# Optimization experiments

Measured on AMD Instinct MI355X. Metric: run time of the kernel, lower is better.

The kernel has to match this reference:

```python
import jax, jax.numpy as jnp
import numpy as np

IN_C = 128
HID = 128
LEAF = 50000
N0, W = 100000, 16
N1, N2 = 25000, 5000
E1, E2 = 500000, 100000


def setup_inputs() -> dict:
    key = jax.random.key(0)
    ks = jax.random.split(key, 16)
    emb = jax.random.normal(ks[0], (LEAF, IN_C), jnp.float32) * 0.02
    emb = emb.at[0].set(0.0)  # padding_idx=0
    inp = {
        "x": jax.random.randint(ks[1], (N0, W), 0, LEAF),
        "src1": jax.random.randint(ks[2], (E1,), 0, N0),
        "dst1": jax.random.randint(ks[3], (E1,), 0, N1),
        "src2": jax.random.randint(ks[4], (E2,), 0, N1),
        "dst2": jax.random.randint(ks[5], (E2,), 0, N2),
        "n1": N1,
        "n2": N2,
        "emb": emb,
        "ln_g": jnp.ones((IN_C,), jnp.float32),
        "ln_b": jnp.zeros((IN_C,), jnp.float32),
        "Wl1": jax.random.normal(ks[6], (HID, IN_C), jnp.float32) * 0.05,
        "bl1": jnp.zeros((HID,), jnp.float32),
        "Wr1": jax.random.normal(ks[7], (HID, IN_C), jnp.float32) * 0.05,
        "Wl2": jax.random.normal(ks[8], (HID, HID), jnp.float32) * 0.05,
        "bl2": jnp.zeros((HID,), jnp.float32),
        "Wr2": jax.random.normal(ks[9], (HID, HID), jnp.float32) * 0.05,
    }
    return inp


def _layernorm(h, g, b, eps=1e-5):
    mu = jnp.mean(h, axis=-1, keepdims=True)
    var = jnp.mean(jnp.square(h - mu), axis=-1, keepdims=True)
    return (h - mu) * jax.lax.rsqrt(var + eps) * g + b


def _sage_conv(h, src, dst, n_tgt, Wl, bl, Wr):
    # bipartite SAGEConv with mean aggregation (PyG default):
    # out = lin_l(mean_j h[src_j -> i]) + lin_r(h[:n_tgt])
    msg = h[src]  # [E, C] irregular gather
    agg = jax.ops.segment_sum(msg, dst, num_segments=n_tgt)
    cnt = jax.ops.segment_sum(jnp.ones((src.shape[0],), h.dtype), dst, num_segments=n_tgt)
    mean = agg / jnp.maximum(cnt, 1.0)[:, None]
    return mean @ Wl.T + bl + h[:n_tgt] @ Wr.T


def reference(x, src1, dst1, src2, dst2, n1, n2, emb, ln_g, ln_b,
              Wl1, bl1, Wr1, Wl2, bl2, Wr2):
    h = jnp.sum(emb[x], axis=1)               # [N0, C] embedding-bag sum
    h = jax.nn.relu(_layernorm(h, ln_g, ln_b))
    h = _sage_conv(h, src1, dst1, n1, Wl1, bl1, Wr1)
    h = jax.nn.relu(h)                        # dropout: eval mode -> identity
    h = _sage_conv(h, src2, dst2, n2, Wl2, bl2, Wr2)
    return h
```

## Files before the change

### kernel.cpp

```cpp
#include <hip/hip_runtime.h>

#define C 128
#define LDSPAD 136
#define CAP 64

typedef unsigned int uint;
typedef unsigned short ushort;
typedef __attribute__((ext_vector_type(8))) short bf16x8;
typedef __attribute__((ext_vector_type(4))) float f32x4;

__device__ __forceinline__ float bf_lo(uint u) { return __uint_as_float(u << 16); }
__device__ __forceinline__ float bf_hi(uint u) { return __uint_as_float(u & 0xffff0000u); }
__device__ __forceinline__ uint f2bf(float f) {
  uint u = __float_as_uint(f);
  return (u + 0x7fffu + ((u >> 16) & 1u)) >> 16;
}

__global__ __launch_bounds__(256) void k_prep(
    const float4* __restrict__ emb, ushort4* __restrict__ embh, int n4,
    const float4* __restrict__ w0, const float4* __restrict__ w1,
    const float4* __restrict__ w2, const float4* __restrict__ w3,
    ushort4* __restrict__ wb, int nw4each,
    int4* __restrict__ zb, int nz4) {
  int i = blockIdx.x * blockDim.x + threadIdx.x;
  if (i < n4) {
    float4 f = emb[i];
    ushort4 o = {(ushort)f2bf(f.x), (ushort)f2bf(f.y), (ushort)f2bf(f.z), (ushort)f2bf(f.w)};
    embh[i] = o;
  }
  if (i < 4 * nw4each) {
    int m = i / nw4each;
    int j = i - m * nw4each;
    const float4* w = (m == 0) ? w0 : (m == 1) ? w1 : (m == 2) ? w2 : w3;
    float4 f = w[j];
    ushort4 o = {(ushort)f2bf(f.x), (ushort)f2bf(f.y), (ushort)f2bf(f.z), (ushort)f2bf(f.w)};
    wb[i] = o;
  }
  if (i < nz4) {
    int4 z = {0, 0, 0, 0};
    zb[i] = z;
  }
}

__global__ __launch_bounds__(256) void k_embed_bucket(
    const int* __restrict__ x, const ushort* __restrict__ emb,
    const float* __restrict__ g, const float* __restrict__ b,
    ushort* __restrict__ h, int n0,
    const int* __restrict__ src1, const int* __restrict__ dst1,
    int* __restrict__ cnt1, int* __restrict__ slots1, int e1,
    const int* __restrict__ src2, const int* __restrict__ dst2,
    int* __restrict__ cnt2, int* __restrict__ slots2, int e2,
    int bucketBlocks) {
  if (blockIdx.x < bucketBlocks) {
    int i = blockIdx.x * blockDim.x + threadIdx.x;
    if (i < e1) {
      int d = dst1[i];
      int p = atomicAdd(&cnt1[d], 1);
      if (p < CAP) slots1[d * CAP + p] = src1[i];
    } else if (i < e1 + e2) {
      int j = i - e1;
      int d = dst2[j];
      int p = atomicAdd(&cnt2[d], 1);
      if (p < CAP) slots2[d * CAP + p] = src2[j];
    }
    return;
  }
  int node = (blockIdx.x - bucketBlocks) * 4 + (threadIdx.x >> 6);
  int lane = threadIdx.x & 63;
  if (node >= n0) return;
  int grp = lane >> 5, sub = lane & 31;
  int xv = x[(size_t)node * 16 + (lane & 15)];
  float s0 = 0.f, s1 = 0.f, s2 = 0.f, s3 = 0.f;
#pragma unroll
  for (int w = 0; w < 16; w += 2) {
    int tok = __shfl(xv, w + grp, 64);
    uint2 u = ((const uint2*)(emb + (size_t)tok * C))[sub];
    s0 += bf_lo(u.x); s1 += bf_hi(u.x); s2 += bf_lo(u.y); s3 += bf_hi(u.y);
  }
  s0 += __shfl_xor(s0, 32, 64);
  s1 += __shfl_xor(s1, 32, 64);
  s2 += __shfl_xor(s2, 32, 64);
  s3 += __shfl_xor(s3, 32, 64);
  float red = s0 + s1 + s2 + s3;
#pragma unroll
  for (int off = 16; off; off >>= 1) red += __shfl_xor(red, off, 64);
  float mu = red * (1.f / C);
  float c0 = s0 - mu, c1 = s1 - mu, c2 = s2 - mu, c3 = s3 - mu;
  float sq = c0 * c0 + c1 * c1 + c2 * c2 + c3 * c3;
#pragma unroll
  for (int off = 16; off; off >>= 1) sq += __shfl_xor(sq, off, 64);
  float rs = rsqrtf(sq * (1.f / C) + 1e-5f);
  float4 gg = ((const float4*)g)[sub];
  float4 bb = ((const float4*)b)[sub];
  float o0 = fmaxf(c0 * rs * gg.x + bb.x, 0.f);
  float o1 = fmaxf(c1 * rs * gg.y + bb.y, 0.f);
  float o2 = fmaxf(c2 * rs * gg.z + bb.z, 0.f);
  float o3 = fmaxf(c3 * rs * gg.w + bb.w, 0.f);
  if (grp == 0) {
    ushort4 o = {(ushort)f2bf(o0), (ushort)f2bf(o1), (ushort)f2bf(o2), (ushort)f2bf(o3)};
    ((ushort4*)(h + (size_t)node * C))[sub] = o;
  }
}

template <bool RELU, bool BF16OUT>
__global__ __launch_bounds__(512) void k_conv(
    const int* __restrict__ cntArr, const int* __restrict__ slots,
    const ushort* __restrict__ h, const ushort* __restrict__ Wlb,
    const float* __restrict__ bl, const ushort* __restrict__ Wrb,
    void* __restrict__ outp, int ntgt) {
  __shared__ ushort smean[16 * LDSPAD];
  int wave = threadIdx.x >> 6;
  int lane = threadIdx.x & 63;
  int grp = lane >> 5, sub = lane & 31;
  int mbase = blockIdx.x * 16;
  int nl = wave * 2 + grp;
  int node = mbase + nl;

  int truecnt = (node < ntgt) ? cntArr[node] : 0;
  int cnt = min(truecnt, CAP);
  const int* sl = slots + (size_t)(node < ntgt ? node : 0) * CAP;
  int ev = (sub < cnt) ? sl[sub] : 0;
  int ev2 = (sub + 32 < cnt) ? sl[sub + 32] : 0;
  int dmax = max(cnt, __shfl_xor(cnt, 32, 64));
  int half = grp * 32;
  float s0 = 0.f, s1 = 0.f, s2 = 0.f, s3 = 0.f;
  for (int d = 0; d < dmax; d += 8) {
#pragma unroll
    for (int k = 0; k < 8; ++k) {
      int dk = d + k;
      int e = (dk < 32) ? __shfl(ev, half + dk, 64) : __shfl(ev2, half + dk - 32, 64);
      uint2 u = ((const uint2*)(h + (size_t)e * C))[sub];
      uint msk = (dk < cnt) ? 0xffffffffu : 0u;
      u.x &= msk; u.y &= msk;
      s0 += bf_lo(u.x); s1 += bf_hi(u.x); s2 += bf_lo(u.y); s3 += bf_hi(u.y);
    }
  }
  float sc = 1.f / (float)max(truecnt, 1);
  ushort4 o = {(ushort)f2bf(s0 * sc), (ushort)f2bf(s1 * sc),
               (ushort)f2bf(s2 * sc), (ushort)f2bf(s3 * sc)};
  *(ushort4*)(smean + nl * LDSPAD + sub * 4) = o;
  __syncthreads();

  int r16 = lane & 15;
  int quad = lane >> 4;
  int koff = quad * 8;
  bf16x8 am[4], ah[4];
  int hr = min(mbase + r16, ntgt - 1);
  const ushort* hrow = h + (size_t)hr * C;
#pragma unroll
  for (int kc = 0; kc < 4; ++kc) {
    am[kc] = *(const bf16x8*)(smean + r16 * LDSPAD + kc * 32 + koff);
    ah[kc] = *(const bf16x8*)(hrow + kc * 32 + koff);
  }
  int nbase = wave * 16;
  float bias = bl[nbase + r16];
  f32x4 acc = {bias, bias, bias, bias};
  const ushort* wlrow = Wlb + (size_t)(nbase + r16) * C;
  const ushort* wrrow = Wrb + (size_t)(nbase + r16) * C;
#pragma unroll
  for (int kc = 0; kc < 4; ++kc) {
    bf16x8 wl = *(const bf16x8*)(wlrow + kc * 32 + koff);
    acc = __builtin_amdgcn_mfma_f32_16x16x32_bf16(am[kc], wl, acc, 0, 0, 0);
    bf16x8 wr = *(const bf16x8*)(wrrow + kc * 32 + koff);
    acc = __builtin_amdgcn_mfma_f32_16x16x32_bf16(ah[kc], wr, acc, 0, 0, 0);
  }
#pragma unroll
  for (int r = 0; r < 4; ++r) {
    int row = mbase + quad * 4 + r;
    if (row < ntgt) {
      float v = acc[r];
      if (RELU) v = fmaxf(v, 0.f);
      if (BF16OUT)
        ((ushort*)outp)[(size_t)row * C + nbase + r16] = (ushort)f2bf(v);
      else
        ((float*)outp)[(size_t)row * C + nbase + r16] = v;
    }
  }
}

extern "C" void kernel_launch(void* const* d_in, const int* in_sizes, int n_in,
                              void* d_out, int out_size, void* d_ws, size_t ws_size,
                              hipStream_t stream) {
  const int*   x    = (const int*)d_in[0];
  const int*   src1 = (const int*)d_in[1];
  const int*   dst1 = (const int*)d_in[2];
  const int*   src2 = (const int*)d_in[3];
  const int*   dst2 = (const int*)d_in[4];
  const float* emb  = (const float*)d_in[7];
  const float* ln_g = (const float*)d_in[8];
  const float* ln_b = (const float*)d_in[9];
  const float* Wl1  = (const float*)d_in[10];
  const float* bl1  = (const float*)d_in[11];
  const float* Wr1  = (const float*)d_in[12];
  const float* Wl2  = (const float*)d_in[13];
  const float* bl2  = (const float*)d_in[14];
  const float* Wr2  = (const float*)d_in[15];

  const int N0 = in_sizes[0] / 16;
  const int E1 = in_sizes[1];
  const int E2 = in_sizes[3];
  const int N1 = 25000;
  const int N2 = 5000;
  const int LEAF_ELEMS = in_sizes[7];
  const int W_ELEMS = C * C;

  char* ws = (char*)d_ws;
  size_t off = 0;
  auto alloc = [&](size_t bytes) {
    char* p = ws + off;
    off += (bytes + 255) & ~(size_t)255;
    return p;
  };
  ushort* embh   = (ushort*)alloc((size_t)LEAF_ELEMS * 2);
  ushort* h0     = (ushort*)alloc((size_t)N0 * C * 2);
  ushort* h1     = (ushort*)alloc((size_t)N1 * C * 2);
  ushort* wb     = (ushort*)alloc((size_t)4 * W_ELEMS * 2);
  int*    slots1 = (int*)alloc((size_t)N1 * CAP * 4);
  int*    slots2 = (int*)alloc((size_t)N2 * CAP * 4);
  char*   zbase  = ws + off;
  int*    cnt1   = (int*)alloc((size_t)N1 * 4);
  int*    cnt2   = (int*)alloc((size_t)N2 * 4);
  size_t  zbytes = (size_t)((ws + off) - zbase);

  float* out = (float*)d_out;
  ushort* Wl1b = wb;
  ushort* Wr1b = wb + W_ELEMS;
  ushort* Wl2b = wb + 2 * W_ELEMS;
  ushort* Wr2b = wb + 3 * W_ELEMS;

  {
    int n4 = LEAF_ELEMS / 4;
    int nw4each = W_ELEMS / 4;
    int nz4 = (int)(zbytes / 16);
    k_prep<<<(n4 + 255) / 256, 256, 0, stream>>>(
        (const float4*)emb, (ushort4*)embh, n4,
        (const float4*)Wl1, (const float4*)Wr1, (const float4*)Wl2, (const float4*)Wr2,
        (ushort4*)wb, nw4each, (int4*)zbase, nz4);
  }

  {
    int bucketBlocks = (E1 + E2 + 255) / 256;
    int embBlocks = (N0 + 3) / 4;
    k_embed_bucket<<<bucketBlocks + embBlocks, 256, 0, stream>>>(
        x, embh, ln_g, ln_b, h0, N0,
        src1, dst1, cnt1, slots1, E1,
        src2, dst2, cnt2, slots2, E2, bucketBlocks);
  }

  k_conv<true, true><<<(N1 + 15) / 16, 512, 0, stream>>>(
      cnt1, slots1, h0, Wl1b, bl1, Wr1b, h1, N1);

  k_conv<false, false><<<(N2 + 15) / 16, 512, 0, stream>>>(
      cnt2, slots2, h1, Wl2b, bl2, Wr2b, out, N2);
}
```

Before: 230.9 us.

## Fuse all stages into one persistent cooperative kernel with grid syncs

Replaces the four separate launches (prep, embed+bucket, two convs) with a single cooperative persistent kernel that uses grid-stride loops and grid.sync between phases. This removes per-launch overhead and inter-kernel gaps. It also makes the edge bucketing and the embedding phase share the same threads instead of separate blocks. The cost is grid-wide barriers, occupancy capped by launch bounds, and a host occupancy query on every call.

```diff
diff --git a/kernel.cpp b/kernel.cpp
--- a/kernel.cpp
+++ b/kernel.cpp
@@ -1,4 +1,7 @@
 #include <hip/hip_runtime.h>
+#include <hip/hip_cooperative_groups.h>
+
+namespace cg = cooperative_groups;
 
 #define C 128
 #define LDSPAD 136
@@ -16,240 +19,252 @@
   return (u + 0x7fffu + ((u >> 16) & 1u)) >> 16;
 }
 
-__global__ __launch_bounds__(256) void k_prep(
-    const float4* __restrict__ emb, ushort4* __restrict__ embh, int n4,
-    const float4* __restrict__ w0, const float4* __restrict__ w1,
-    const float4* __restrict__ w2, const float4* __restrict__ w3,
-    ushort4* __restrict__ wb, int nw4each,
-    int4* __restrict__ zb, int nz4) {
-  int i = blockIdx.x * blockDim.x + threadIdx.x;
-  if (i < n4) {
-    float4 f = emb[i];
-    ushort4 o = {(ushort)f2bf(f.x), (ushort)f2bf(f.y), (ushort)f2bf(f.z), (ushort)f2bf(f.w)};
-    embh[i] = o;
-  }
-  if (i < 4 * nw4each) {
-    int m = i / nw4each;
-    int j = i - m * nw4each;
-    const float4* w = (m == 0) ? w0 : (m == 1) ? w1 : (m == 2) ? w2 : w3;
-    float4 f = w[j];
-    ushort4 o = {(ushort)f2bf(f.x), (ushort)f2bf(f.y), (ushort)f2bf(f.z), (ushort)f2bf(f.w)};
-    wb[i] = o;
-  }
-  if (i < nz4) {
-    int4 z = {0, 0, 0, 0};
-    zb[i] = z;
-  }
-}
-
-__global__ __launch_bounds__(256) void k_embed_bucket(
-    const int* __restrict__ x, const ushort* __restrict__ emb,
-    const float* __restrict__ g, const float* __restrict__ b,
-    ushort* __restrict__ h, int n0,
-    const int* __restrict__ src1, const int* __restrict__ dst1,
-    int* __restrict__ cnt1, int* __restrict__ slots1, int e1,
-    const int* __restrict__ src2, const int* __restrict__ dst2,
-    int* __restrict__ cnt2, int* __restrict__ slots2, int e2,
-    int bucketBlocks) {
-  if (blockIdx.x < bucketBlocks) {
-    int i = blockIdx.x * blockDim.x + threadIdx.x;
-    if (i < e1) {
-      int d = dst1[i];
-      int p = atomicAdd(&cnt1[d], 1);
-      if (p < CAP) slots1[d * CAP + p] = src1[i];
-    } else if (i < e1 + e2) {
-      int j = i - e1;
-      int d = dst2[j];
-      int p = atomicAdd(&cnt2[d], 1);
-      if (p < CAP) slots2[d * CAP + p] = src2[j];
-    }
-    return;
-  }
-  int node = (blockIdx.x - bucketBlocks) * 4 + (threadIdx.x >> 6);
-  int lane = threadIdx.x & 63;
-  if (node >= n0) return;
-  int grp = lane >> 5, sub = lane & 31;
-  int xv = x[(size_t)node * 16 + (lane & 15)];
-  float s0 = 0.f, s1 = 0.f, s2 = 0.f, s3 = 0.f;
-#pragma unroll
-  for (int w = 0; w < 16; w += 2) {
-    int tok = __shfl(xv, w + grp, 64);
-    uint2 u = ((const uint2*)(emb + (size_t)tok * C))[sub];
-    s0 += bf_lo(u.x); s1 += bf_hi(u.x); s2 += bf_lo(u.y); s3 += bf_hi(u.y);
-  }
-  s0 += __shfl_xor(s0, 32, 64);
-  s1 += __shfl_xor(s1, 32, 64);
-  s2 += __shfl_xor(s2, 32, 64);
-  s3 += __shfl_xor(s3, 32, 64);
-  float red = s0 + s1 + s2 + s3;
-#pragma unroll
-  for (int off = 16; off; off >>= 1) red += __shfl_xor(red, off, 64);
-  float mu = red * (1.f / C);
-  float c0 = s0 - mu, c1 = s1 - mu, c2 = s2 - mu, c3 = s3 - mu;
-  float sq = c0 * c0 + c1 * c1 + c2 * c2 + c3 * c3;
-#pragma unroll
-  for (int off = 16; off; off >>= 1) sq += __shfl_xor(sq, off, 64);
-  float rs = rsqrtf(sq * (1.f / C) + 1e-5f);
-  float4 gg = ((const float4*)g)[sub];
-  float4 bb = ((const float4*)b)[sub];
-  float o0 = fmaxf(c0 * rs * gg.x + bb.x, 0.f);
-  float o1 = fmaxf(c1 * rs * gg.y + bb.y, 0.f);
-  float o2 = fmaxf(c2 * rs * gg.z + bb.z, 0.f);
-  float o3 = fmaxf(c3 * rs * gg.w + bb.w, 0.f);
-  if (grp == 0) {
-    ushort4 o = {(ushort)f2bf(o0), (ushort)f2bf(o1), (ushort)f2bf(o2), (ushort)f2bf(o3)};
-    ((ushort4*)(h + (size_t)node * C))[sub] = o;
-  }
-}
+struct Params {
+  const int* x;
+  const float* emb;
+  const float* ln_g;
+  const float* ln_b;
+  const int* src1; const int* dst1;
+  const int* src2; const int* dst2;
+  const float* Wl1; const float* bl1; const float* Wr1;
+  const float* Wl2; const float* bl2; const float* Wr2;
+  ushort* embh; ushort* h0; ushort* h1; ushort* wb;
+  int* cnt1; int* slots1; int* cnt2; int* slots2;
+  int4* zbase; int nz4;
+  float* out;
+  int n0, e1, e2, n1, n2, leafElems;
+};
 
 template <bool RELU, bool BF16OUT>
-__global__ __launch_bounds__(512) void k_conv(
+__device__ __forceinline__ void conv_phase(
     const int* __restrict__ cntArr, const int* __restrict__ slots,
     const ushort* __restrict__ h, const ushort* __restrict__ Wlb,
     const float* __restrict__ bl, const ushort* __restrict__ Wrb,
-    void* __restrict__ outp, int ntgt) {
-  __shared__ ushort smean[16 * LDSPAD];
+    void* __restrict__ outp, int ntgt, ushort* smean) {
   int wave = threadIdx.x >> 6;
   int lane = threadIdx.x & 63;
   int grp = lane >> 5, sub = lane & 31;
-  int mbase = blockIdx.x * 16;
-  int nl = wave * 2 + grp;
-  int node = mbase + nl;
-
-  int truecnt = (node < ntgt) ? cntArr[node] : 0;
-  int cnt = min(truecnt, CAP);
-  const int* sl = slots + (size_t)(node < ntgt ? node : 0) * CAP;
-  int ev = (sub < cnt) ? sl[sub] : 0;
-  int ev2 = (sub + 32 < cnt) ? sl[sub + 32] : 0;
-  int dmax = max(cnt, __shfl_xor(cnt, 32, 64));
-  int half = grp * 32;
-  float s0 = 0.f, s1 = 0.f, s2 = 0.f, s3 = 0.f;
-  for (int d = 0; d < dmax; d += 8) {
-#pragma unroll
-    for (int k = 0; k < 8; ++k) {
-      int dk = d + k;
-      int e = (dk < 32) ? __shfl(ev, half + dk, 64) : __shfl(ev2, half + dk - 32, 64);
-      uint2 u = ((const uint2*)(h + (size_t)e * C))[sub];
-      uint msk = (dk < cnt) ? 0xffffffffu : 0u;
-      u.x &= msk; u.y &= msk;
-      s0 += bf_lo(u.x); s1 += bf_hi(u.x); s2 += bf_lo(u.y); s3 += bf_hi(u.y);
-    }
-  }
-  float sc = 1.f / (float)max(truecnt, 1);
-  ushort4 o = {(ushort)f2bf(s0 * sc), (ushort)f2bf(s1 * sc),
-               (ushort)f2bf(s2 * sc), (ushort)f2bf(s3 * sc)};
-  *(ushort4*)(smean + nl * LDSPAD + sub * 4) = o;
-  __syncthreads();
-
   int r16 = lane & 15;
   int quad = lane >> 4;
   int koff = quad * 8;
-  bf16x8 am[4], ah[4];
-  int hr = min(mbase + r16, ntgt - 1);
-  const ushort* hrow = h + (size_t)hr * C;
-#pragma unroll
-  for (int kc = 0; kc < 4; ++kc) {
-    am[kc] = *(const bf16x8*)(smean + r16 * LDSPAD + kc * 32 + koff);
-    ah[kc] = *(const bf16x8*)(hrow + kc * 32 + koff);
+  int ntiles = (ntgt + 15) >> 4;
+  for (int t = blockIdx.x; t < ntiles; t += gridDim.x) {
+    int mbase = t * 16;
+    int nl = wave * 2 + grp;
+    int node = mbase + nl;
+    __syncthreads();
+    int truecnt = (node < ntgt) ? cntArr[node] : 0;
+    int cnt = min(truecnt, CAP);
+    const int* sl = slots + (size_t)(node < ntgt ? node : 0) * CAP;
+    int ev = (sub < cnt) ? sl[sub] : 0;
+    int ev2 = (sub + 32 < cnt) ? sl[sub + 32] : 0;
+    int dmax = max(cnt, __shfl_xor(cnt, 32, 64));
+    int half = grp * 32;
+    float s0 = 0.f, s1 = 0.f, s2 = 0.f, s3 = 0.f;
+    for (int d = 0; d < dmax; d += 8) {
+#pragma unroll
+      for (int k = 0; k < 8; ++k) {
+        int dk = d + k;
+        int e = (dk < 32) ? __shfl(ev, half + dk, 64) : __shfl(ev2, half + dk - 32, 64);
+        uint2 u = ((const uint2*)(h + (size_t)e * C))[sub];
+        uint msk = (dk < cnt) ? 0xffffffffu : 0u;
+        u.x &= msk; u.y &= msk;
+        s0 += bf_lo(u.x); s1 += bf_hi(u.x); s2 += bf_lo(u.y); s3 += bf_hi(u.y);
+      }
+    }
+    float sc = 1.f / (float)max(truecnt, 1);
+    ushort4 o = {(ushort)f2bf(s0 * sc), (ushort)f2bf(s1 * sc),
+                 (ushort)f2bf(s2 * sc), (ushort)f2bf(s3 * sc)};
+    *(ushort4*)(smean + nl * LDSPAD + sub * 4) = o;
+    __syncthreads();
+    bf16x8 am[4], ah[4];
+    int hr = min(mbase + r16, ntgt - 1);
+    const ushort* hrow = h + (size_t)hr * C;
+#pragma unroll
+    for (int kc = 0; kc < 4; ++kc) {
+      am[kc] = *(const bf16x8*)(smean + r16 * LDSPAD + kc * 32 + koff);
+      ah[kc] = *(const bf16x8*)(hrow + kc * 32 + koff);
+    }
+    int nbase = wave * 16;
+    float bias = bl[nbase + r16];
+    f32x4 acc = {bias, bias, bias, bias};
+    const ushort* wlrow = Wlb + (size_t)(nbase + r16) * C;
+    const ushort* wrrow = Wrb + (size_t)(nbase + r16) * C;
+#pragma unroll
+    for (int kc = 0; kc < 4; ++kc) {
+      bf16x8 wl = *(const bf16x8*)(wlrow + kc * 32 + koff);
+      acc = __builtin_amdgcn_mfma_f32_16x16x32_bf16(am[kc], wl, acc, 0, 0, 0);
+      bf16x8 wr = *(const bf16x8*)(wrrow + kc * 32 + koff);
+      acc = __builtin_amdgcn_mfma_f32_16x16x32_bf16(ah[kc], wr, acc, 0, 0, 0);
+    }
+#pragma unroll
+    for (int r = 0; r < 4; ++r) {
+      int row = mbase + quad * 4 + r;
+      if (row < ntgt) {
+        float v = acc[r];
+        if (RELU) v = fmaxf(v, 0.f);
+        if (BF16OUT)
+          ((ushort*)outp)[(size_t)row * C + nbase + r16] = (ushort)f2bf(v);
+        else
+          ((float*)outp)[(size_t)row * C + nbase + r16] = v;
+      }
+    }
   }
-  int nbase = wave * 16;
-  float bias = bl[nbase + r16];
-  f32x4 acc = {bias, bias, bias, bias};
-  const ushort* wlrow = Wlb + (size_t)(nbase + r16) * C;
-  const ushort* wrrow = Wrb + (size_t)(nbase + r16) * C;
-#pragma unroll
-  for (int kc = 0; kc < 4; ++kc) {
-    bf16x8 wl = *(const bf16x8*)(wlrow + kc * 32 + koff);
-    acc = __builtin_amdgcn_mfma_f32_16x16x32_bf16(am[kc], wl, acc, 0, 0, 0);
-    bf16x8 wr = *(const bf16x8*)(wrrow + kc * 32 + koff);
-    acc = __builtin_amdgcn_mfma_f32_16x16x32_bf16(ah[kc], wr, acc, 0, 0, 0);
+}
+
+__global__ __launch_bounds__(512, 4) void k_all(Params p) {
+  cg::grid_group grid = cg::this_grid();
+  __shared__ ushort smean[16 * LDSPAD];
+  const int tid = threadIdx.x;
+  const int gtid = blockIdx.x * 512 + tid;
+  const int gsz = gridDim.x * 512;
+
+  {
+    int n4 = p.leafElems / 4;
+    const float4* ef = (const float4*)p.emb;
+    ushort4* eo = (ushort4*)p.embh;
+    for (int i = gtid; i < n4; i += gsz) {
+      float4 f = ef[i];
+      ushort4 o = {(ushort)f2bf(f.x), (ushort)f2bf(f.y), (ushort)f2bf(f.z), (ushort)f2bf(f.w)};
+      eo[i] = o;
+    }
+    int nw4 = (C * C) / 4;
+    ushort4* wo = (ushort4*)p.wb;
+    for (int i = gtid; i < 4 * nw4; i += gsz) {
+      int m = i / nw4;
+      int j = i - m * nw4;
+      const float4* w = (m == 0) ? (const float4*)p.Wl1
+                      : (m == 1) ? (const float4*)p.Wr1
+                      : (m == 2) ? (const float4*)p.Wl2
+                                 : (const float4*)p.Wr2;
+      float4 f = w[j];
+      ushort4 o = {(ushort)f2bf(f.x), (ushort)f2bf(f.y), (ushort)f2bf(f.z), (ushort)f2bf(f.w)};
+      wo[i] = o;
+    }
+    int4 z = {0, 0, 0, 0};
+    for (int i = gtid; i < p.nz4; i += gsz) p.zbase[i] = z;
   }
-#pragma unroll
-  for (int r = 0; r < 4; ++r) {
-    int row = mbase + quad * 4 + r;
-    if (row < ntgt) {
-      float v = acc[r];
-      if (RELU) v = fmaxf(v, 0.f);
-      if (BF16OUT)
-        ((ushort*)outp)[(size_t)row * C + nbase + r16] = (ushort)f2bf(v);
-      else
-        ((float*)outp)[(size_t)row * C + nbase + r16] = v;
+  __threadfence();
+  grid.sync();
+
+  {
+    int etot = p.e1 + p.e2;
+    for (int i = gtid; i < etot; i += gsz) {
+      if (i < p.e1) {
+        int d = p.dst1[i];
+        int pos = atomicAdd(&p.cnt1[d], 1);
+        if (pos < CAP) p.slots1[d * CAP + pos] = p.src1[i];
+      } else {
+        int j = i - p.e1;
+        int d = p.dst2[j];
+        int pos = atomicAdd(&p.cnt2[d], 1);
+        if (pos < CAP) p.slots2[d * CAP + pos] = p.src2[j];
+      }
+    }
+    int lane = tid & 63;
+    int grp = lane >> 5, sub = lane & 31;
+    int gwave = blockIdx.x * 8 + (tid >> 6);
+    int nwaves = gridDim.x * 8;
+    for (int node = gwave; node < p.n0; node += nwaves) {
+      int xv = p.x[(size_t)node * 16 + (lane & 15)];
+      float s0 = 0.f, s1 = 0.f, s2 = 0.f, s3 = 0.f;
+#pragma unroll
+      for (int w = 0; w < 16; w += 2) {
+        int tok = __shfl(xv, w + grp, 64);
+        uint2 u = ((const uint2*)(p.embh + (size_t)tok * C))[sub];
+        s0 += bf_lo(u.x); s1 += bf_hi(u.x); s2 += bf_lo(u.y); s3 += bf_hi(u.y);
+      }
+      s0 += __shfl_xor(s0, 32, 64);
+      s1 += __shfl_xor(s1, 32, 64);
+      s2 += __shfl_xor(s2, 32, 64);
+      s3 += __shfl_xor(s3, 32, 64);
+      float red = s0 + s1 + s2 + s3;
+#pragma unroll
+      for (int off = 16; off; off >>= 1) red += __shfl_xor(red, off, 64);
+      float mu = red * (1.f / C);
+      float c0 = s0 - mu, c1 = s1 - mu, c2 = s2 - mu, c3 = s3 - mu;
+      float sq = c0 * c0 + c1 * c1 + c2 * c2 + c3 * c3;
+#pragma unroll
+      for (int off = 16; off; off >>= 1) sq += __shfl_xor(sq, off, 64);
+      float rs = rsqrtf(sq * (1.f / C) + 1e-5f);
+      float4 gg = ((const float4*)p.ln_g)[sub];
+      float4 bb = ((const float4*)p.ln_b)[sub];
+      float o0 = fmaxf(c0 * rs * gg.x + bb.x, 0.f);
+      float o1 = fmaxf(c1 * rs * gg.y + bb.y, 0.f);
+      float o2 = fmaxf(c2 * rs * gg.z + bb.z, 0.f);
+      float o3 = fmaxf(c3 * rs * gg.w + bb.w, 0.f);
+      if (grp == 0) {
+        ushort4 o = {(ushort)f2bf(o0), (ushort)f2bf(o1), (ushort)f2bf(o2), (ushort)f2bf(o3)};
+        ((ushort4*)(p.h0 + (size_t)node * C))[sub] = o;
+      }
     }
   }
+  __threadfence();
+  grid.sync();
+
+  const int W_ELEMS = C * C;
+  conv_phase<true, true>(p.cnt1, p.slots1, p.h0, p.wb, p.bl1, p.wb + W_ELEMS,
+                         p.h1, p.n1, smean);
+  __threadfence();
+  grid.sync();
+
+  conv_phase<false, false>(p.cnt2, p.slots2, p.h1, p.wb + 2 * W_ELEMS, p.bl2,
+                           p.wb + 3 * W_ELEMS, p.out, p.n2, smean);
 }
 
 extern "C" void kernel_launch(void* const* d_in, const int* in_sizes, int n_in,
                               void* d_out, int out_size, void* d_ws, size_t ws_size,
                               hipStream_t stream) {
-  const int*   x    = (const int*)d_in[0];
-  const int*   src1 = (const int*)d_in[1];
-  const int*   dst1 = (const int*)d_in[2];
-  const int*   src2 = (const int*)d_in[3];
-  const int*   dst2 = (const int*)d_in[4];
-  const float* emb  = (const float*)d_in[7];
-  const float* ln_g = (const float*)d_in[8];
-  const float* ln_b = (const float*)d_in[9];
-  const float* Wl1  = (const float*)d_in[10];
-  const float* bl1  = (const float*)d_in[11];
-  const float* Wr1  = (const float*)d_in[12];
-  const float* Wl2  = (const float*)d_in[13];
-  const float* bl2  = (const float*)d_in[14];
-  const float* Wr2  = (const float*)d_in[15];
-
-  const int N0 = in_sizes[0] / 16;
-  const int E1 = in_sizes[1];
-  const int E2 = in_sizes[3];
-  const int N1 = 25000;
-  const int N2 = 5000;
-  const int LEAF_ELEMS = in_sizes[7];
+  Params p;
+  p.x    = (const int*)d_in[0];
+  p.src1 = (const int*)d_in[1];
+  p.dst1 = (const int*)d_in[2];
+  p.src2 = (const int*)d_in[3];
+  p.dst2 = (const int*)d_in[4];
+  p.emb  = (const float*)d_in[7];
+  p.ln_g = (const float*)d_in[8];
+  p.ln_b = (const float*)d_in[9];
+  p.Wl1  = (const float*)d_in[10];
+  p.bl1  = (const float*)d_in[11];
+  p.Wr1  = (const float*)d_in[12];
+  p.Wl2  = (const float*)d_in[13];
+  p.bl2  = (const float*)d_in[14];
+  p.Wr2  = (const float*)d_in[15];
+
+  p.n0 = in_sizes[0] / 16;
+  p.e1 = in_sizes[1];
+  p.e2 = in_sizes[3];
+  p.n1 = 25000;
+  p.n2 = 5000;
+  p.leafElems = in_sizes[7];
   const int W_ELEMS = C * C;
 
   char* ws = (char*)d_ws;
   size_t off = 0;
   auto alloc = [&](size_t bytes) {
-    char* p = ws + off;
+    char* ptr = ws + off;
     off += (bytes + 255) & ~(size_t)255;
-    return p;
+    return ptr;
   };
-  ushort* embh   = (ushort*)alloc((size_t)LEAF_ELEMS * 2);
-  ushort* h0     = (ushort*)alloc((size_t)N0 * C * 2);
-  ushort* h1     = (ushort*)alloc((size_t)N1 * C * 2);
-  ushort* wb     = (ushort*)alloc((size_t)4 * W_ELEMS * 2);
-  int*    slots1 = (int*)alloc((size_t)N1 * CAP * 4);
-  int*    slots2 = (int*)alloc((size_t)N2 * CAP * 4);
-  char*   zbase  = ws + off;
-  int*    cnt1   = (int*)alloc((size_t)N1 * 4);
-  int*    cnt2   = (int*)alloc((size_t)N2 * 4);
-  size_t  zbytes = (size_t)((ws + off) - zbase);
-
-  float* out = (float*)d_out;
-  ushort* Wl1b = wb;
-  ushort* Wr1b = wb + W_ELEMS;
-  ushort* Wl2b = wb + 2 * W_ELEMS;
-  ushort* Wr2b = wb + 3 * W_ELEMS;
-
-  {
-    int n4 = LEAF_ELEMS / 4;
-    int nw4each = W_ELEMS / 4;
-    int nz4 = (int)(zbytes / 16);
-    k_prep<<<(n4 + 255) / 256, 256, 0, stream>>>(
-        (const float4*)emb, (ushort4*)embh, n4,
-        (const float4*)Wl1, (const float4*)Wr1, (const float4*)Wl2, (const float4*)Wr2,
-        (ushort4*)wb, nw4each, (int4*)zbase, nz4);
-  }
-
-  {
-    int bucketBlocks = (E1 + E2 + 255) / 256;
-    int embBlocks = (N0 + 3) / 4;
-    k_embed_bucket<<<bucketBlocks + embBlocks, 256, 0, stream>>>(
-        x, embh, ln_g, ln_b, h0, N0,
-        src1, dst1, cnt1, slots1, E1,
-        src2, dst2, cnt2, slots2, E2, bucketBlocks);
-  }
-
-  k_conv<true, true><<<(N1 + 15) / 16, 512, 0, stream>>>(
-      cnt1, slots1, h0, Wl1b, bl1, Wr1b, h1, N1);
-
-  k_conv<false, false><<<(N2 + 15) / 16, 512, 0, stream>>>(
-      cnt2, slots2, h1, Wl2b, bl2, Wr2b, out, N2);
-}
+  p.embh   = (ushort*)alloc((size_t)p.leafElems * 2);
+  p.h0     = (ushort*)alloc((size_t)p.n0 * C * 2);
+  p.h1     = (ushort*)alloc((size_t)p.n1 * C * 2);
+  p.wb     = (ushort*)alloc((size_t)4 * W_ELEMS * 2);
+  p.slots1 = (int*)alloc((size_t)p.n1 * CAP * 4);
+  p.slots2 = (int*)alloc((size_t)p.n2 * CAP * 4);
+  char* zbase = ws + off;
+  p.cnt1   = (int*)alloc((size_t)p.n1 * 4);
+  p.cnt2   = (int*)alloc((size_t)p.n2 * 4);
+  size_t zbytes = (size_t)((ws + off) - zbase);
+  p.zbase = (int4*)zbase;
+  p.nz4 = (int)(zbytes / 16);
+  p.out = (float*)d_out;
+
+  int maxBlk = 0;
+  hipError_t e = hipOccupancyMaxActiveBlocksPerMultiprocessor(&maxBlk, k_all, 512, 0);
+  if (e != hipSuccess || maxBlk < 1) maxBlk = 1;
+  int nblk = maxBlk * 256;
+  if (nblk > 2048) nblk = 2048;
+  void* args[] = {&p};
+  hipLaunchCooperativeKernel((void*)k_all, dim3(nblk), dim3(512), args, 0, stream);
+}
```

Measured after the change: 525.8 us. 2.28x slower.
